# Optimization experiments

Hardware: AMD Instinct MI355X
Metric: run time of the kernel (lower is better)

## Reference

```python
import jax, jax.numpy as jnp
import numpy as np

LAYER_START = 4   # module init arg layer_start
WIN = 2           # module init arg context_window_size
EPS = 1e-8        # clamp in cosine_similarity_torch


def setup_inputs() -> dict:
    key = jax.random.key(0)
    k1, k2 = jax.random.split(key)
    L_all, B, S, D = 13, 8, 512, 768  # BERT-base: embeddings + 12 layers
    hidden_states = jax.random.normal(k1, (L_all, B, S, D), dtype=jnp.float32)
    lengths = jax.random.randint(k2, (B,), S // 2, S + 1)
    attention_mask = (jnp.arange(S)[None, :] < lengths[:, None]).astype(jnp.int32)
    return {"hidden_states": hidden_states, "attention_mask": attention_mask}


def _wk_forward(hidden_states, attention_mask):
    # hidden_states: (L_all, B, S, D) -> keep layers from LAYER_START on
    x = jnp.transpose(hidden_states, (1, 0, 2, 3))[:, LAYER_START:]  # (B, L, S, D)
    B, L, S, D = x.shape
    feats = jnp.transpose(x, (0, 2, 1, 3))  # (B, S, L, D) per-token layer features

    # ---- unify_token: per-token, QR over windowed layer embeddings ----
    aligns, novs = [], []
    for k in range(L):  # small fixed loop over layers (9 iters)
        left = list(range(k - WIN, k)) if k >= WIN else []
        right = list(range(k + 1, min(k + WIN + 1, L)))
        idx = np.array(left + right + [k])
        n = idx.size  # = window_matrix.size(0) in torch
        A = jnp.swapaxes(feats[:, :, idx, :], -1, -2)  # (B, S, D, n) = window_matrix.T
        _, R = jnp.linalg.qr(A)                        # R: (B, S, n, n)
        r = R[..., :, -1]                              # last column of R
        Rsub = R[..., :-1, :-1]
        # columns of Rsub normalized along dim 0, mean over columns, dot R[:-1,-1]
        Rhat = Rsub / jnp.linalg.norm(Rsub, axis=-2, keepdims=True)
        align = jnp.sum(jnp.mean(Rhat, axis=-1) * R[..., :-1, -1], axis=-1)
        align = align / jnp.linalg.norm(r[..., :-1], axis=-1)
        align = 1.0 / (align * (n * 2))
        nov = jnp.abs(r[..., -1]) / jnp.linalg.norm(r, axis=-1)
        aligns.append(align)
        novs.append(nov)
    align = jnp.stack(aligns, axis=-1)  # (B, S, L)
    nov = jnp.stack(novs, axis=-1)      # (B, S, L)
    align = align / jnp.sum(align, axis=-1, keepdims=True)
    nov = nov / jnp.sum(nov, axis=-1, keepdims=True)
    alpha = align + nov
    alpha = alpha / jnp.sum(alpha, axis=-1, keepdims=True)
    token_emb = jnp.einsum('bsl,bsld->bsd', alpha, feats)  # per-token embedding

    # ---- unify_sentence: variance of sub-diagonal cosine sims across layers ----
    norms = jnp.linalg.norm(feats, axis=-1)  # (B, S, L)
    c = jnp.sum(feats[:, :, 1:] * feats[:, :, :-1], axis=-1)
    c = c / jnp.clip(norms[:, :, 1:] * norms[:, :, :-1], EPS)  # (B, S, L-1)
    var_tok = jnp.var(c, axis=-1, ddof=1)  # torch.var is unbiased

    lengths = jnp.sum(attention_mask, axis=1) - 1  # unmask_num
    valid = jnp.arange(S)[None, :] < lengths[:, None]
    v = jnp.where(valid, var_tok, 0.0)
    v = v / jnp.sum(v, axis=-1, keepdims=True)
    return jnp.einsum('bs,bsd->bd', v, token_emb)  # (B, D)


def reference(hidden_states, attention_mask):
    return _wk_forward(hidden_states, attention_mask)
```

## Files before the change

### kernel.cpp

```cpp
#include <hip/hip_runtime.h>

#define B_ 8
#define S_ 512
#define D_ 768
#define LAYER0 4
#define LSTRIDE (8*512*768)
#define LSTRIDE4 (LSTRIDE/4)
#define SCH 32
#define CW (S_/SCH)

__device__ const int QI9[45] = {0,0,0,0,0,0,0,0,0, 1,1,1,1,1,1,1,1, 2,2,2,2,2,2,2,
                                3,3,3,3,3,3, 4,4,4,4,4, 5,5,5,5, 6,6,6, 7,7, 8};
__device__ const int QJ9[45] = {0,1,2,3,4,5,6,7,8, 1,2,3,4,5,6,7,8, 2,3,4,5,6,7,8,
                                3,4,5,6,7,8, 4,5,6,7,8, 5,6,7,8, 6,7,8, 7,8, 8};

__device__ __forceinline__ float dot4(const float4& a, const float4& b) {
  return fmaf(a.x, b.x, fmaf(a.y, b.y, fmaf(a.z, b.z, a.w * b.w)));
}

__global__ __launch_bounds__(192) void wk_token(const float* __restrict__ hid,
                                                float* __restrict__ wte,
                                                float* __restrict__ wv) {
  const int token = blockIdx.x;
  const int b = token >> 9;
  const int s = token & (S_ - 1);
  const int t = threadIdx.x;

  __shared__ float pgl[192][25];
  __shared__ float red[2][24][6];
  __shared__ float Gl[9][9];
  __shared__ float s_align[9], s_nov[9];

  const float4* base = (const float4*)(hid + ((((size_t)LAYER0) * B_ + b) * S_ + s) * D_) + t;
  float4 f[9];
#pragma unroll
  for (int l = 0; l < 9; ++l) f[l] = base[(size_t)l * LSTRIDE4];

  float pg2[21];
  {
    int q = 0;
#pragma unroll
    for (int i = 0; i < 9; ++i) {
#pragma unroll
      for (int j = i; j < 9; ++j) {
        float p = dot4(f[i], f[j]);
        if (q < 24) pgl[t][q] = p;
        else pg2[q - 24] = p;
        ++q;
      }
    }
  }
  __syncthreads();

  {
    const int q = t & 31, sub = t >> 5;
    if (q < 24) {
      float acc = 0.f;
#pragma unroll
      for (int r = 0; r < 32; ++r) acc += pgl[sub * 32 + r][q];
      red[0][q][sub] = acc;
    }
  }
  __syncthreads();

#pragma unroll
  for (int q = 0; q < 21; ++q) pgl[t][q] = pg2[q];
  if (t < 24) {
    float acc = 0.f;
#pragma unroll
    for (int u = 0; u < 6; ++u) acc += red[0][t][u];
    const int i = QI9[t], j = QJ9[t];
    Gl[i][j] = acc; Gl[j][i] = acc;
  }
  __syncthreads();

  {
    const int q = t & 31, sub = t >> 5;
    if (q < 21) {
      float acc = 0.f;
#pragma unroll
      for (int r = 0; r < 32; ++r) acc += pgl[sub * 32 + r][q];
      red[1][q][sub] = acc;
    }
  }
  __syncthreads();
  if (t < 21) {
    float acc = 0.f;
#pragma unroll
    for (int u = 0; u < 6; ++u) acc += red[1][t][u];
    const int i = QI9[24 + t], j = QJ9[24 + t];
    Gl[i][j] = acc; Gl[j][i] = acc;
  }
  __syncthreads();

  if (t < 9) {
    const int k = t;
    int nb[4]; int m = 0;
    if (k >= 2) { nb[m++] = k - 2; nb[m++] = k - 1; }
    if (k + 1 < 9) nb[m++] = k + 1;
    if (k + 2 < 9) nb[m++] = k + 2;
    const int n = m + 1;

    float g[4], Lc[4][4], tv[4];
    for (int i = 0; i < m; ++i) g[i] = Gl[nb[i]][k];

    for (int i = 0; i < m; ++i) {
      for (int j = 0; j <= i; ++j) {
        float sum = Gl[nb[i]][nb[j]];
        for (int p2 = 0; p2 < j; ++p2) sum -= Lc[i][p2] * Lc[j][p2];
        Lc[i][j] = (i == j) ? sqrtf(sum) : sum / Lc[j][j];
      }
    }
    float s2 = 0.f;
    for (int i = 0; i < m; ++i) {
      float sum = g[i];
      for (int p2 = 0; p2 < i; ++p2) sum -= Lc[i][p2] * tv[p2];
      tv[i] = sum / Lc[i][i];
      s2 += tv[i] * tv[i];
    }
    float ar = 0.f;
    for (int i = 0; i < m; ++i) ar += g[i] / sqrtf(Gl[nb[i]][nb[i]]);
    ar /= (float)m;

    float align = sqrtf(s2) / (ar * (2.0f * (float)n));
    float Gkk = Gl[k][k];
    float nov = sqrtf(fmaxf(Gkk - s2, 0.f)) / sqrtf(Gkk);
    s_align[k] = align;
    s_nov[k] = nov;
  }
  if (t == 9) {
    float sc = 0.f, sc2 = 0.f;
    for (int i = 0; i < 8; ++i) {
      float nn = sqrtf(Gl[i][i]) * sqrtf(Gl[i + 1][i + 1]);
      nn = fmaxf(nn, 1e-8f);
      float ci = Gl[i][i + 1] / nn;
      sc += ci; sc2 += ci * ci;
    }
    float mean = sc * 0.125f;
    wv[token] = (sc2 - 8.f * mean * mean) * (1.f / 7.f);
  }
  __syncthreads();

  float sa = 0.f, sn = 0.f;
#pragma unroll
  for (int l = 0; l < 9; ++l) { sa += s_align[l]; sn += s_nov[l]; }
  float alpha[9]; float ss = 0.f;
#pragma unroll
  for (int l = 0; l < 9; ++l) { alpha[l] = s_align[l] / sa + s_nov[l] / sn; ss += alpha[l]; }
  const float inv = 1.f / ss;
  float t0 = 0.f, t1 = 0.f, t2 = 0.f, t3 = 0.f;
#pragma unroll
  for (int l = 0; l < 9; ++l) {
    float a = alpha[l] * inv;
    t0 += a * f[l].x;
    t1 += a * f[l].y;
    t2 += a * f[l].z;
    t3 += a * f[l].w;
  }
  ((float4*)(wte + (size_t)token * D_))[t] = make_float4(t0, t1, t2, t3);
}

__global__ __launch_bounds__(192) void wk_pool_partial(const float* __restrict__ wte,
                                                       const float* __restrict__ wv,
                                                       const int* __restrict__ mask,
                                                       float* __restrict__ P,
                                                       float* __restrict__ Pw) {
  const int b = blockIdx.x / SCH;
  const int c = blockIdx.x % SCH;
  const int t = threadIdx.x;
  const int lane = t & 63, wid = t >> 6;

  __shared__ float vl[CW];
  __shared__ int redm[3];
  __shared__ int s_len;

  int acc = 0;
  if (t < S_) acc = mask[b * S_ + t];
  {
    int i2 = t + 192; acc += mask[b * S_ + i2];
    int i3 = t + 384; if (i3 < S_) acc += mask[b * S_ + i3];
  }
  acc += __shfl_xor(acc, 32); acc += __shfl_xor(acc, 16); acc += __shfl_xor(acc, 8);
  acc += __shfl_xor(acc, 4);  acc += __shfl_xor(acc, 2);  acc += __shfl_xor(acc, 1);
  if (lane == 0) redm[wid] = acc;
  if (t < CW) vl[t] = wv[b * S_ + c * CW + t];
  __syncthreads();
  if (t == 0) s_len = redm[0] + redm[1] + redm[2] - 1;
  __syncthreads();
  const int len = s_len;

  float a0 = 0.f, a1 = 0.f, a2 = 0.f, a3 = 0.f;
  const float4* base = (const float4*)(wte + ((size_t)b * S_ + c * CW) * D_) + t;
  float wsum = 0.f;
#pragma unroll 4
  for (int s = 0; s < CW; ++s) {
    float w = (c * CW + s < len) ? vl[s] : 0.f;
    wsum += w;
    float4 p = base[s * (D_ / 4)];
    a0 += w * p.x; a1 += w * p.y; a2 += w * p.z; a3 += w * p.w;
  }
  ((float4*)(P + (size_t)blockIdx.x * D_))[t] = make_float4(a0, a1, a2, a3);
  if (t == 0) Pw[blockIdx.x] = wsum;
}

__global__ __launch_bounds__(256) void wk_pool_final(const float* __restrict__ P,
                                                     const float* __restrict__ Pw,
                                                     float* __restrict__ out) {
  const int i = blockIdx.x * 256 + threadIdx.x;
  const int b = i / (D_ / 4);
  const int d4 = i % (D_ / 4);
  float n0 = 0.f, n1 = 0.f, n2 = 0.f, n3 = 0.f, den = 0.f;
#pragma unroll
  for (int c = 0; c < SCH; ++c) {
    float4 p = ((const float4*)P)[((size_t)b * SCH + c) * (D_ / 4) + d4];
    n0 += p.x; n1 += p.y; n2 += p.z; n3 += p.w;
    den += Pw[b * SCH + c];
  }
  float inv = 1.f / den;
  ((float4*)out)[i] = make_float4(n0 * inv, n1 * inv, n2 * inv, n3 * inv);
}

extern "C" void kernel_launch(void* const* d_in, const int* in_sizes, int n_in,
                              void* d_out, int out_size, void* d_ws, size_t ws_size,
                              hipStream_t stream) {
  const float* hid = (const float*)d_in[0];
  const int* mask = (const int*)d_in[1];
  float* out = (float*)d_out;

  float* wte = (float*)d_ws;
  float* wv  = wte + (size_t)B_ * S_ * D_;
  float* P   = wv + B_ * S_;
  float* Pw  = P + (size_t)B_ * SCH * D_;

  wk_token<<<B_ * S_, 192, 0, stream>>>(hid, wte, wv);
  wk_pool_partial<<<B_ * SCH, 192, 0, stream>>>(wte, wv, mask, P, Pw);
  wk_pool_final<<<(B_ * (D_ / 4) + 255) / 256, 256, 0, stream>>>(P, Pw, out);
}
```

Before: 63.13 us.

## Use single-wavefront blocks per token with shuffle reductions and pre-weighted outputs

The token kernel now runs one 64-lane wavefront per token, each lane holding 27 float4 values. That lets the Gram reduction finish in a single shared-memory pass, and the alpha and variance values are broadcast with wave shuffles instead of shared memory and extra barriers. The mask length is computed inside the token kernel and the per-token variance weight is folded into the stored embedding, so the pooling kernel only does plain sums. The cost is much higher register pressure per thread, which may lower occupancy, plus some redundant mask reads in every block.

```diff
diff --git a/kernel.cpp b/kernel.cpp
--- a/kernel.cpp
+++ b/kernel.cpp
@@ -4,8 +4,7 @@
 #define S_ 512
 #define D_ 768
 #define LAYER0 4
-#define LSTRIDE (8*512*768)
-#define LSTRIDE4 (LSTRIDE/4)
+#define LSTRIDE4 (8*512*768/4)
 #define SCH 32
 #define CW (S_/SCH)
 
@@ -18,81 +17,65 @@
   return fmaf(a.x, b.x, fmaf(a.y, b.y, fmaf(a.z, b.z, a.w * b.w)));
 }
 
-__global__ __launch_bounds__(192) void wk_token(const float* __restrict__ hid,
-                                                float* __restrict__ wte,
-                                                float* __restrict__ wv) {
+__global__ __launch_bounds__(64) void wk_token(const float* __restrict__ hid,
+                                               const int* __restrict__ mask,
+                                               float* __restrict__ wte,
+                                               float* __restrict__ wv) {
   const int token = blockIdx.x;
   const int b = token >> 9;
   const int s = token & (S_ - 1);
   const int t = threadIdx.x;
 
-  __shared__ float pgl[192][25];
-  __shared__ float red[2][24][6];
-  __shared__ float Gl[9][9];
-  __shared__ float s_align[9], s_nov[9];
-
-  const float4* base = (const float4*)(hid + ((((size_t)LAYER0) * B_ + b) * S_ + s) * D_) + t;
-  float4 f[9];
-#pragma unroll
-  for (int l = 0; l < 9; ++l) f[l] = base[(size_t)l * LSTRIDE4];
-
-  float pg2[21];
+  __shared__ float pgl[64][46];
+  __shared__ float Gsym[81];
+
+  int mlen;
+  {
+    const int4* mp = (const int4*)(mask + b * S_);
+    int4 m1 = mp[t];
+    int4 m2 = mp[t + 64];
+    int acc = m1.x + m1.y + m1.z + m1.w + m2.x + m2.y + m2.z + m2.w;
+    acc += __shfl_xor(acc, 32); acc += __shfl_xor(acc, 16);
+    acc += __shfl_xor(acc, 8);  acc += __shfl_xor(acc, 4);
+    acc += __shfl_xor(acc, 2);  acc += __shfl_xor(acc, 1);
+    mlen = acc - 1;
+  }
+
+  const float4* base = (const float4*)hid
+      + (((size_t)LAYER0 * B_ + b) * S_ + s) * (D_ / 4) + t;
+  float4 f[27];
+#pragma unroll
+  for (int l = 0; l < 9; ++l) {
+#pragma unroll
+    for (int c = 0; c < 3; ++c) f[l * 3 + c] = base[(size_t)l * LSTRIDE4 + c * 64];
+  }
+
   {
     int q = 0;
 #pragma unroll
     for (int i = 0; i < 9; ++i) {
 #pragma unroll
       for (int j = i; j < 9; ++j) {
-        float p = dot4(f[i], f[j]);
-        if (q < 24) pgl[t][q] = p;
-        else pg2[q - 24] = p;
+        float d = dot4(f[i * 3], f[j * 3])
+                + dot4(f[i * 3 + 1], f[j * 3 + 1])
+                + dot4(f[i * 3 + 2], f[j * 3 + 2]);
+        pgl[t][q] = d;
         ++q;
       }
     }
   }
   __syncthreads();
 
-  {
-    const int q = t & 31, sub = t >> 5;
-    if (q < 24) {
-      float acc = 0.f;
-#pragma unroll
-      for (int r = 0; r < 32; ++r) acc += pgl[sub * 32 + r][q];
-      red[0][q][sub] = acc;
-    }
+  if (t < 45) {
+    float tot = 0.f;
+#pragma unroll
+    for (int r = 0; r < 64; r += 2) tot += pgl[r][t] + pgl[r + 1][t];
+    Gsym[QI9[t] * 9 + QJ9[t]] = tot;
+    Gsym[QJ9[t] * 9 + QI9[t]] = tot;
   }
   __syncthreads();
 
-#pragma unroll
-  for (int q = 0; q < 21; ++q) pgl[t][q] = pg2[q];
-  if (t < 24) {
-    float acc = 0.f;
-#pragma unroll
-    for (int u = 0; u < 6; ++u) acc += red[0][t][u];
-    const int i = QI9[t], j = QJ9[t];
-    Gl[i][j] = acc; Gl[j][i] = acc;
-  }
-  __syncthreads();
-
-  {
-    const int q = t & 31, sub = t >> 5;
-    if (q < 21) {
-      float acc = 0.f;
-#pragma unroll
-      for (int r = 0; r < 32; ++r) acc += pgl[sub * 32 + r][q];
-      red[1][q][sub] = acc;
-    }
-  }
-  __syncthreads();
-  if (t < 21) {
-    float acc = 0.f;
-#pragma unroll
-    for (int u = 0; u < 6; ++u) acc += red[1][t][u];
-    const int i = QI9[24 + t], j = QJ9[24 + t];
-    Gl[i][j] = acc; Gl[j][i] = acc;
-  }
-  __syncthreads();
-
+  float align = 0.f, nov = 0.f, var = 0.f;
   if (t < 9) {
     const int k = t;
     int nb[4]; int m = 0;
@@ -102,105 +85,95 @@
     const int n = m + 1;
 
     float g[4], Lc[4][4], tv[4];
-    for (int i = 0; i < m; ++i) g[i] = Gl[nb[i]][k];
+    for (int i = 0; i < m; ++i) g[i] = Gsym[nb[i] * 9 + k];
 
     for (int i = 0; i < m; ++i) {
       for (int j = 0; j <= i; ++j) {
-        float sum = Gl[nb[i]][nb[j]];
-        for (int p2 = 0; p2 < j; ++p2) sum -= Lc[i][p2] * Lc[j][p2];
+        float sum = Gsym[nb[i] * 9 + nb[j]];
+        for (int p = 0; p < j; ++p) sum -= Lc[i][p] * Lc[j][p];
         Lc[i][j] = (i == j) ? sqrtf(sum) : sum / Lc[j][j];
       }
     }
     float s2 = 0.f;
     for (int i = 0; i < m; ++i) {
       float sum = g[i];
-      for (int p2 = 0; p2 < i; ++p2) sum -= Lc[i][p2] * tv[p2];
+      for (int p = 0; p < i; ++p) sum -= Lc[i][p] * tv[p];
       tv[i] = sum / Lc[i][i];
       s2 += tv[i] * tv[i];
     }
     float ar = 0.f;
-    for (int i = 0; i < m; ++i) ar += g[i] / sqrtf(Gl[nb[i]][nb[i]]);
+    for (int i = 0; i < m; ++i) ar += g[i] / sqrtf(Gsym[nb[i] * 9 + nb[i]]);
     ar /= (float)m;
 
-    float align = sqrtf(s2) / (ar * (2.0f * (float)n));
-    float Gkk = Gl[k][k];
-    float nov = sqrtf(fmaxf(Gkk - s2, 0.f)) / sqrtf(Gkk);
-    s_align[k] = align;
-    s_nov[k] = nov;
+    align = sqrtf(s2) / (ar * (2.0f * (float)n));
+    float Gkk = Gsym[k * 9 + k];
+    nov = sqrtf(fmaxf(Gkk - s2, 0.f)) / sqrtf(Gkk);
   }
   if (t == 9) {
     float sc = 0.f, sc2 = 0.f;
     for (int i = 0; i < 8; ++i) {
-      float nn = sqrtf(Gl[i][i]) * sqrtf(Gl[i + 1][i + 1]);
+      float nn = sqrtf(Gsym[i * 9 + i]) * sqrtf(Gsym[(i + 1) * 9 + i + 1]);
       nn = fmaxf(nn, 1e-8f);
-      float ci = Gl[i][i + 1] / nn;
+      float ci = Gsym[i * 9 + i + 1] / nn;
       sc += ci; sc2 += ci * ci;
     }
     float mean = sc * 0.125f;
-    wv[token] = (sc2 - 8.f * mean * mean) * (1.f / 7.f);
-  }
-  __syncthreads();
+    var = (sc2 - 8.f * mean * mean) * (1.f / 7.f);
+  }
+
+  float w = __shfl(var, 9);
+  if (s >= mlen) w = 0.f;
 
   float sa = 0.f, sn = 0.f;
 #pragma unroll
-  for (int l = 0; l < 9; ++l) { sa += s_align[l]; sn += s_nov[l]; }
-  float alpha[9]; float ss = 0.f;
-#pragma unroll
-  for (int l = 0; l < 9; ++l) { alpha[l] = s_align[l] / sa + s_nov[l] / sn; ss += alpha[l]; }
-  const float inv = 1.f / ss;
-  float t0 = 0.f, t1 = 0.f, t2 = 0.f, t3 = 0.f;
-#pragma unroll
-  for (int l = 0; l < 9; ++l) {
-    float a = alpha[l] * inv;
-    t0 += a * f[l].x;
-    t1 += a * f[l].y;
-    t2 += a * f[l].z;
-    t3 += a * f[l].w;
-  }
-  ((float4*)(wte + (size_t)token * D_))[t] = make_float4(t0, t1, t2, t3);
-}
-
-__global__ __launch_bounds__(192) void wk_pool_partial(const float* __restrict__ wte,
-                                                       const float* __restrict__ wv,
-                                                       const int* __restrict__ mask,
-                                                       float* __restrict__ P,
-                                                       float* __restrict__ Pw) {
-  const int b = blockIdx.x / SCH;
-  const int c = blockIdx.x % SCH;
+  for (int i = 0; i < 9; ++i) { sa += __shfl(align, i); sn += __shfl(nov, i); }
+  float alpha = align / sa + nov / sn;
+  float ss = 0.f;
+#pragma unroll
+  for (int i = 0; i < 9; ++i) ss += __shfl(alpha, i);
+
+  const float inv = w / ss;
+  float a9[9];
+#pragma unroll
+  for (int l = 0; l < 9; ++l) a9[l] = __shfl(alpha, l) * inv;
+
+  float4* o = (float4*)wte + (size_t)token * (D_ / 4) + t;
+#pragma unroll
+  for (int c = 0; c < 3; ++c) {
+    float4 acc = make_float4(0.f, 0.f, 0.f, 0.f);
+#pragma unroll
+    for (int l = 0; l < 9; ++l) {
+      float a = a9[l];
+      float4 p = f[l * 3 + c];
+      acc.x += a * p.x; acc.y += a * p.y; acc.z += a * p.z; acc.w += a * p.w;
+    }
+    o[c * 64] = acc;
+  }
+  if (t == 0) wv[token] = w;
+}
+
+__global__ __launch_bounds__(192) void wk_pool(const float* __restrict__ wte,
+                                               const float* __restrict__ wv,
+                                               float* __restrict__ P,
+                                               float* __restrict__ Pw) {
+  const int b = blockIdx.x >> 5;
+  const int c = blockIdx.x & 31;
   const int t = threadIdx.x;
-  const int lane = t & 63, wid = t >> 6;
-
-  __shared__ float vl[CW];
-  __shared__ int redm[3];
-  __shared__ int s_len;
-
-  int acc = 0;
-  if (t < S_) acc = mask[b * S_ + t];
-  {
-    int i2 = t + 192; acc += mask[b * S_ + i2];
-    int i3 = t + 384; if (i3 < S_) acc += mask[b * S_ + i3];
-  }
-  acc += __shfl_xor(acc, 32); acc += __shfl_xor(acc, 16); acc += __shfl_xor(acc, 8);
-  acc += __shfl_xor(acc, 4);  acc += __shfl_xor(acc, 2);  acc += __shfl_xor(acc, 1);
-  if (lane == 0) redm[wid] = acc;
-  if (t < CW) vl[t] = wv[b * S_ + c * CW + t];
-  __syncthreads();
-  if (t == 0) s_len = redm[0] + redm[1] + redm[2] - 1;
-  __syncthreads();
-  const int len = s_len;
-
-  float a0 = 0.f, a1 = 0.f, a2 = 0.f, a3 = 0.f;
-  const float4* base = (const float4*)(wte + ((size_t)b * S_ + c * CW) * D_) + t;
-  float wsum = 0.f;
+
+  float4 a = make_float4(0.f, 0.f, 0.f, 0.f);
+  const float4* base = (const float4*)wte + ((size_t)b * S_ + c * CW) * (D_ / 4) + t;
 #pragma unroll 4
-  for (int s = 0; s < CW; ++s) {
-    float w = (c * CW + s < len) ? vl[s] : 0.f;
-    wsum += w;
-    float4 p = base[s * (D_ / 4)];
-    a0 += w * p.x; a1 += w * p.y; a2 += w * p.z; a3 += w * p.w;
-  }
-  ((float4*)(P + (size_t)blockIdx.x * D_))[t] = make_float4(a0, a1, a2, a3);
-  if (t == 0) Pw[blockIdx.x] = wsum;
+  for (int sl = 0; sl < CW; ++sl) {
+    float4 p = base[sl * (D_ / 4)];
+    a.x += p.x; a.y += p.y; a.z += p.z; a.w += p.w;
+  }
+  ((float4*)P)[(size_t)blockIdx.x * (D_ / 4) + t] = a;
+  if (t == 0) {
+    float ws = 0.f;
+#pragma unroll
+    for (int i = 0; i < CW; ++i) ws += wv[b * S_ + c * CW + i];
+    Pw[blockIdx.x] = ws;
+  }
 }
 
 __global__ __launch_bounds__(256) void wk_pool_final(const float* __restrict__ P,
@@ -232,7 +205,7 @@
   float* P   = wv + B_ * S_;
   float* Pw  = P + (size_t)B_ * SCH * D_;
 
-  wk_token<<<B_ * S_, 192, 0, stream>>>(hid, wte, wv);
-  wk_pool_partial<<<B_ * SCH, 192, 0, stream>>>(wte, wv, mask, P, Pw);
+  wk_token<<<B_ * S_, 64, 0, stream>>>(hid, mask, wte, wv);
+  wk_pool<<<B_ * SCH, 192, 0, stream>>>(wte, wv, P, Pw);
   wk_pool_final<<<(B_ * (D_ / 4) + 255) / 256, 256, 0, stream>>>(P, Pw, out);
 }
```

Result: faster. 52.32 us (-17.1%).
